# Optimization experiments

Hardware: AMD Instinct MI355X
Metric: run time of the kernel (lower is better)

Reference implementation:

```python
import jax, jax.numpy as jnp
import numpy as np


def setup_inputs() -> dict:
    key = jax.random.key(0)
    ks = jax.random.split(key, 4)
    B, Tq, Tv, D = 8, 256, 512, 256  # decoder_dim = D = 256
    query = jax.random.normal(ks[0], (B, Tq, D), dtype=jnp.float32)
    value = jax.random.normal(ks[1], (B, Tv, D), dtype=jnp.float32)
    W1 = jax.random.normal(ks[2], (D, D), dtype=jnp.float32) * (1.0 / np.sqrt(D))
    b1 = jnp.zeros((D,), dtype=jnp.float32)
    W2 = jax.random.normal(ks[3], (D, D), dtype=jnp.float32) * (1.0 / np.sqrt(D))
    b2 = jnp.zeros((D,), dtype=jnp.float32)
    return {"query": query, "value": value, "W1": W1, "b1": b1, "W2": W2, "b2": b2}


def reference(query, value, W1, b1, W2, b2):
    # Dense projections: [B,Tq,D], [B,Tv,D]
    q = jnp.einsum('bqd,de->bqe', query, W1) + b1
    v = jnp.einsum('bvd,de->bve', value, W2) + b2
    # Additive (Bahdanau) score: broadcast tanh then reduce over feature dim
    # score: [B,Tq,Tv]  (intermediate [B,Tq,Tv,D] is the fusion target)
    score = jnp.tanh(q[:, :, None, :] + v[:, None, :, :]).sum(axis=-1)
    alignment = jax.nn.softmax(score, axis=-1)  # [B,Tq,Tv]
    context = jnp.einsum('bqv,bvd->bqd', alignment, value)  # [B,Tq,D]
    context = jnp.concatenate([context, query], axis=-1)  # [B,Tq,2D]
    alignment_t = jnp.transpose(alignment, (0, 2, 1))  # [B,Tv,Tq]
    return context, alignment_t
```

## Files before the change

### kernel.cpp

```cpp
#include <hip/hip_runtime.h>

#define B_  8
#define TQ  256
#define TV  512
#define DD  256
#define ALGS 520

__device__ __forceinline__ float fast_exp2(float x) {
#if __has_builtin(__builtin_amdgcn_exp2f)
  return __builtin_amdgcn_exp2f(x);
#else
  return __exp2f(x);
#endif
}
__device__ __forceinline__ float fast_rcp(float x) {
#if __has_builtin(__builtin_amdgcn_rcpf)
  return __builtin_amdgcn_rcpf(x);
#else
  return 1.0f / x;
#endif
}

__global__ __launch_bounds__(256) void proj_fused(
    const float* __restrict__ query, const float* __restrict__ value,
    const float* __restrict__ W1, const float* __restrict__ b1,
    const float* __restrict__ W2, const float* __restrict__ b2,
    float* __restrict__ qp, float* __restrict__ vp, float scale) {
  __shared__ float As[2][32][64];
  __shared__ float Bs[2][32][64];
  const int t  = threadIdx.x;
  const int rt = blockIdx.x;
  const int bn = blockIdx.y << 6;

  const float* A; const float* W; const float* bias; float* out; int row0;
  if (rt < 32) { row0 = rt << 6;        A = query; W = W1; bias = b1; out = qp; }
  else         { row0 = (rt - 32) << 6; A = value; W = W2; bias = b2; out = vp; }

  const int tx = t & 15, ty = t >> 4;
  const int aar = t >> 3, aac = (t & 7) << 2;
  const int bbr = t >> 4, bbc = (t & 15) << 2;

  float4 ra[2], rb[2];
#pragma unroll
  for (int it = 0; it < 2; ++it) {
    ra[it] = *(const float4*)(A + (size_t)(row0 + (it << 5) + aar) * DD + aac);
    rb[it] = *(const float4*)(W + (size_t)((it << 4) + bbr) * DD + bn + bbc);
  }
#pragma unroll
  for (int it = 0; it < 2; ++it) {
    const int m = (it << 5) + aar;
#pragma unroll
    for (int c = 0; c < 4; ++c) {
      const int k = aac + c;
      As[0][k][m ^ (((k >> 2) & 7) << 2)] = (&ra[it].x)[c];
    }
    *(float4*)&Bs[0][(it << 4) + bbr][bbc] = rb[it];
  }
  __syncthreads();

  float acc[4][4] = {{0.f,0.f,0.f,0.f},{0.f,0.f,0.f,0.f},
                     {0.f,0.f,0.f,0.f},{0.f,0.f,0.f,0.f}};
  int p = 0;

  for (int k0 = 0; k0 < 256; k0 += 32) {
    const bool more = (k0 + 32) < 256;
    if (more) {
#pragma unroll
      for (int it = 0; it < 2; ++it) {
        ra[it] = *(const float4*)(A + (size_t)(row0 + (it << 5) + aar) * DD + k0 + 32 + aac);
        rb[it] = *(const float4*)(W + (size_t)(k0 + 32 + (it << 4) + bbr) * DD + bn + bbc);
      }
    }
#pragma unroll
    for (int k = 0; k < 32; ++k) {
      float4 aq = *(const float4*)&As[p][k][(ty << 2) ^ (((k >> 2) & 7) << 2)];
      float4 bq = *(const float4*)&Bs[p][k][tx << 2];
      acc[0][0] = fmaf(aq.x, bq.x, acc[0][0]); acc[0][1] = fmaf(aq.x, bq.y, acc[0][1]);
      acc[0][2] = fmaf(aq.x, bq.z, acc[0][2]); acc[0][3] = fmaf(aq.x, bq.w, acc[0][3]);
      acc[1][0] = fmaf(aq.y, bq.x, acc[1][0]); acc[1][1] = fmaf(aq.y, bq.y, acc[1][1]);
      acc[1][2] = fmaf(aq.y, bq.z, acc[1][2]); acc[1][3] = fmaf(aq.y, bq.w, acc[1][3]);
      acc[2][0] = fmaf(aq.z, bq.x, acc[2][0]); acc[2][1] = fmaf(aq.z, bq.y, acc[2][1]);
      acc[2][2] = fmaf(aq.z, bq.z, acc[2][2]); acc[2][3] = fmaf(aq.z, bq.w, acc[2][3]);
      acc[3][0] = fmaf(aq.w, bq.x, acc[3][0]); acc[3][1] = fmaf(aq.w, bq.y, acc[3][1]);
      acc[3][2] = fmaf(aq.w, bq.z, acc[3][2]); acc[3][3] = fmaf(aq.w, bq.w, acc[3][3]);
    }
    if (more) {
      const int q = p ^ 1;
#pragma unroll
      for (int it = 0; it < 2; ++it) {
        const int m = (it << 5) + aar;
#pragma unroll
        for (int c = 0; c < 4; ++c) {
          const int k = aac + c;
          As[q][k][m ^ (((k >> 2) & 7) << 2)] = (&ra[it].x)[c];
        }
        *(float4*)&Bs[q][(it << 4) + bbr][bbc] = rb[it];
      }
      __syncthreads();
      p = q;
    }
  }

  float4 bvv = *(const float4*)&bias[bn + (tx << 2)];
#pragma unroll
  for (int r = 0; r < 4; ++r) {
    float4 o;
    o.x = fast_exp2(scale * (acc[r][0] + bvv.x));
    o.y = fast_exp2(scale * (acc[r][1] + bvv.y));
    o.z = fast_exp2(scale * (acc[r][2] + bvv.z));
    o.w = fast_exp2(scale * (acc[r][3] + bvv.w));
    *(float4*)(out + (size_t)(row0 + (ty << 2) + r) * DD + bn + (tx << 2)) = o;
  }
}

__global__ __launch_bounds__(512, 4) void attn_kernel(
    const float* __restrict__ qp, const float* __restrict__ vp,
    const float* __restrict__ value, const float* __restrict__ query,
    float* __restrict__ out1, float* __restrict__ out2) {
  __shared__ float qs[4 * 256];
  __shared__ float alg[4 * ALGS];
  __shared__ float ctxp[8][4][256];

  const int t    = threadIdx.x;
  const int lane = t & 63;
  const int wv   = t >> 6;
  const int jj   = lane >> 2;
  const int dq   = lane & 3;
  const int bb   = blockIdx.x & 7;
  const int i0   = (blockIdx.x >> 3) << 2;

  const float* vpb = vp + (size_t)bb * TV * DD;
  const float* qb  = qp + (size_t)(bb * TQ + i0) * DD;

  if (t < 256) {
    const int qi = t >> 6, qc = (t & 63) << 2;
    *(float4*)&qs[qi * 256 + qc] = *(const float4*)(qb + (size_t)qi * DD + qc);
  }
  __syncthreads();

  const int jb = (wv << 4) + jj;
  const float* vr0 = vpb + (size_t)jb * DD + (dq << 2);
  const float* vr1 = vr0 + 128 * DD;
  const float* vr2 = vr0 + 256 * DD;
  const float* vr3 = vr0 + 384 * DD;
  const float* qlane = qs + (dq << 2);

  float acc[4][4] = {{0.f,0.f,0.f,0.f},{0.f,0.f,0.f,0.f},
                     {0.f,0.f,0.f,0.f},{0.f,0.f,0.f,0.f}};

#pragma unroll 4
  for (int k = 0; k < 16; ++k) {
    const int doff = k << 4;
    float4 q0 = *(const float4*)(qlane + 0 * 256 + doff);
    float4 q1 = *(const float4*)(qlane + 1 * 256 + doff);
    float4 q2 = *(const float4*)(qlane + 2 * 256 + doff);
    float4 q3 = *(const float4*)(qlane + 3 * 256 + doff);
#pragma unroll
    for (int jg = 0; jg < 4; ++jg) {
      const float* vrp = (jg == 0) ? vr0 : (jg == 1) ? vr1 : (jg == 2) ? vr2 : vr3;
      float4 v4 = *(const float4*)(vrp + doff);
#pragma unroll
      for (int i = 0; i < 4; ++i) {
        const float4 q4 = (i == 0) ? q0 : (i == 1) ? q1 : (i == 2) ? q2 : q3;
        float a = q4.x * v4.x, b = q4.y * v4.y;
        float c = q4.z * v4.z, d = q4.w * v4.w;
        float sab = a + b,  scd = c + d;
        float Q1 = fmaf(a, b, sab + 1.f);
        float Q2 = fmaf(c, d, scd + 1.f);
        float N  = fmaf(scd + 2.f, Q1, (sab + 2.f) * Q2);
        acc[i][jg] = fmaf(N, fast_rcp(Q1 * Q2), acc[i][jg]);
      }
    }
  }

#pragma unroll
  for (int i = 0; i < 4; ++i)
#pragma unroll
    for (int jg = 0; jg < 4; ++jg) {
      acc[i][jg] += __shfl_xor(acc[i][jg], 1, 64);
      acc[i][jg] += __shfl_xor(acc[i][jg], 2, 64);
    }
#pragma unroll
  for (int jg = 0; jg < 4; ++jg) {
    float x = (dq == 0) ? acc[0][jg] : (dq == 1) ? acc[1][jg]
            : (dq == 2) ? acc[2][jg] : acc[3][jg];
    alg[dq * ALGS + (jg << 7) + jb] = x;
  }

  const int f4 = (t & 63) << 2;
  const int s  = t >> 6;
  const float* vb  = value + (size_t)bb * TV * DD;
  const float* vsp = vb + (size_t)(s << 6) * DD + f4;

  float4 pv0 = *(const float4*)(vsp + 0 * DD);
  float4 pv1 = *(const float4*)(vsp + 1 * DD);
  float4 pv2 = *(const float4*)(vsp + 2 * DD);
  float4 pv3 = *(const float4*)(vsp + 3 * DD);

  __syncthreads();

  if (wv < 4) {
    float sv[8];
#pragma unroll
    for (int c = 0; c < 8; ++c) sv[c] = alg[wv * ALGS + (c << 6) + lane];
    float mn = sv[0];
#pragma unroll
    for (int c = 1; c < 8; ++c) mn = fminf(mn, sv[c]);
#pragma unroll
    for (int m = 1; m < 64; m <<= 1) mn = fminf(mn, __shfl_xor(mn, m, 64));

    const float CC = 2.8853900817779268f;
    float p[8];
    float sum = 0.f;
#pragma unroll
    for (int c = 0; c < 8; ++c) { p[c] = fast_exp2(CC * (mn - sv[c])); sum += p[c]; }
#pragma unroll
    for (int m = 1; m < 64; m <<= 1) sum += __shfl_xor(sum, m, 64);
    const float inv = fast_rcp(sum);
#pragma unroll
    for (int c = 0; c < 8; ++c) alg[wv * ALGS + (c << 6) + lane] = p[c] * inv;
  }
  __syncthreads();

  {
    const int j = t;
    float4 av = make_float4(alg[j], alg[ALGS + j], alg[2 * ALGS + j], alg[3 * ALGS + j]);
    *(float4*)(out2 + (size_t)(bb * TV + j) * TQ + i0) = av;
  }

  float c4[4][4] = {{0.f,0.f,0.f,0.f},{0.f,0.f,0.f,0.f},
                    {0.f,0.f,0.f,0.f},{0.f,0.f,0.f,0.f}};
  const int jbase = s << 6;
  {
#pragma unroll
    for (int i = 0; i < 4; ++i) {
      float4 ai = *(const float4*)&alg[i * ALGS + jbase];
      c4[i][0] = fmaf(ai.x, pv0.x, c4[i][0]); c4[i][1] = fmaf(ai.x, pv0.y, c4[i][1]);
      c4[i][2] = fmaf(ai.x, pv0.z, c4[i][2]); c4[i][3] = fmaf(ai.x, pv0.w, c4[i][3]);
      c4[i][0] = fmaf(ai.y, pv1.x, c4[i][0]); c4[i][1] = fmaf(ai.y, pv1.y, c4[i][1]);
      c4[i][2] = fmaf(ai.y, pv1.z, c4[i][2]); c4[i][3] = fmaf(ai.y, pv1.w, c4[i][3]);
      c4[i][0] = fmaf(ai.z, pv2.x, c4[i][0]); c4[i][1] = fmaf(ai.z, pv2.y, c4[i][1]);
      c4[i][2] = fmaf(ai.z, pv2.z, c4[i][2]); c4[i][3] = fmaf(ai.z, pv2.w, c4[i][3]);
      c4[i][0] = fmaf(ai.w, pv3.x, c4[i][0]); c4[i][1] = fmaf(ai.w, pv3.y, c4[i][1]);
      c4[i][2] = fmaf(ai.w, pv3.z, c4[i][2]); c4[i][3] = fmaf(ai.w, pv3.w, c4[i][3]);
    }
  }
#pragma unroll 4
  for (int u = 4; u < 64; u += 4) {
    float4 v0 = *(const float4*)(vsp + (size_t)(u + 0) * DD);
    float4 v1 = *(const float4*)(vsp + (size_t)(u + 1) * DD);
    float4 v2 = *(const float4*)(vsp + (size_t)(u + 2) * DD);
    float4 v3 = *(const float4*)(vsp + (size_t)(u + 3) * DD);
#pragma unroll
    for (int i = 0; i < 4; ++i) {
      float4 ai = *(const float4*)&alg[i * ALGS + jbase + u];
      c4[i][0] = fmaf(ai.x, v0.x, c4[i][0]); c4[i][1] = fmaf(ai.x, v0.y, c4[i][1]);
      c4[i][2] = fmaf(ai.x, v0.z, c4[i][2]); c4[i][3] = fmaf(ai.x, v0.w, c4[i][3]);
      c4[i][0] = fmaf(ai.y, v1.x, c4[i][0]); c4[i][1] = fmaf(ai.y, v1.y, c4[i][1]);
      c4[i][2] = fmaf(ai.y, v1.z, c4[i][2]); c4[i][3] = fmaf(ai.y, v1.w, c4[i][3]);
      c4[i][0] = fmaf(ai.z, v2.x, c4[i][0]); c4[i][1] = fmaf(ai.z, v2.y, c4[i][1]);
      c4[i][2] = fmaf(ai.z, v2.z, c4[i][2]); c4[i][3] = fmaf(ai.z, v2.w, c4[i][3]);
      c4[i][0] = fmaf(ai.w, v3.x, c4[i][0]); c4[i][1] = fmaf(ai.w, v3.y, c4[i][1]);
      c4[i][2] = fmaf(ai.w, v3.z, c4[i][2]); c4[i][3] = fmaf(ai.w, v3.w, c4[i][3]);
    }
  }
#pragma unroll
  for (int i = 0; i < 4; ++i)
    *(float4*)&ctxp[s][i][f4] = make_float4(c4[i][0], c4[i][1], c4[i][2], c4[i][3]);
  __syncthreads();

  const float* qg = query + (size_t)(bb * TQ + i0) * DD;
  float* o = out1 + (size_t)(bb * TQ + i0) * (2 * DD);
#pragma unroll
  for (int it = 0; it < 2; ++it) {
    const int slot = t + (it << 9);
    const int ri = slot >> 8;
    const int ff = slot & 255;
    float sum = 0.f;
#pragma unroll
    for (int ss = 0; ss < 8; ++ss) sum += ctxp[ss][ri][ff];
    o[ri * 512 + ff] = sum;
    o[ri * 512 + 256 + ff] = qg[ri * DD + ff];
  }
}

extern "C" void kernel_launch(void* const* d_in, const int* in_sizes, int n_in,
                              void* d_out, int out_size, void* d_ws, size_t ws_size,
                              hipStream_t stream) {
  const float* query = (const float*)d_in[0];
  const float* value = (const float*)d_in[1];
  const float* W1    = (const float*)d_in[2];
  const float* b1    = (const float*)d_in[3];
  const float* W2    = (const float*)d_in[4];
  const float* b2    = (const float*)d_in[5];

  float* out1 = (float*)d_out;
  float* out2 = out1 + (size_t)B_ * TQ * 2 * DD;

  float* qp = (float*)d_ws;
  float* vp = qp + (size_t)B_ * TQ * DD;

  const float SC = 2.8853900817779268f;

  proj_fused<<<dim3(96, 4), 256, 0, stream>>>(query, value, W1, b1, W2, b2, qp, vp, SC);
  attn_kernel<<<dim3(B_ * (TQ / 4)), 512, 0, stream>>>(qp, vp, value, query, out1, out2);
}
```

Measured before the change: 130.9 us.

## Split score computation over feature halves into separate kernel for more parallelism

The fused attention kernel is split in two. The first kernel computes partial tanh-sum scores over half of the feature dimension, using 1024 blocks and a higher occupancy hint, and writes them to workspace. The second kernel sums the two halves, applies softmax and computes the context. The aim is to double the block count for the compute-heavy score phase so that all CUs are filled. The cost is an extra launch plus a partial-score round trip through global memory, and the old monolithic kernel is kept as a fallback when the workspace is too small.

```diff
diff --git a/kernel.cpp b/kernel.cpp
--- a/kernel.cpp
+++ b/kernel.cpp
@@ -113,33 +113,33 @@
   }
 }
 
-__global__ __launch_bounds__(512, 4) void attn_kernel(
+__global__ __launch_bounds__(512, 8) void score_part(
     const float* __restrict__ qp, const float* __restrict__ vp,
-    const float* __restrict__ value, const float* __restrict__ query,
-    float* __restrict__ out1, float* __restrict__ out2) {
-  __shared__ float qs[4 * 256];
+    float* __restrict__ Sp) {
+  __shared__ float qs[4 * 128];
   __shared__ float alg[4 * ALGS];
-  __shared__ float ctxp[8][4][256];
 
   const int t    = threadIdx.x;
   const int lane = t & 63;
   const int wv   = t >> 6;
   const int jj   = lane >> 2;
   const int dq   = lane & 3;
-  const int bb   = blockIdx.x & 7;
-  const int i0   = (blockIdx.x >> 3) << 2;
+  const int bx   = blockIdx.x;
+  const int bb   = bx & 7;
+  const int rest = bx >> 3;
+  const int iblk = rest & 63;
+  const int i0   = iblk << 2;
+  const int dh   = rest >> 6;
+  const int d0   = dh << 7;
 
   const float* vpb = vp + (size_t)bb * TV * DD;
-  const float* qb  = qp + (size_t)(bb * TQ + i0) * DD;
-
-  if (t < 256) {
-    const int qi = t >> 6, qc = (t & 63) << 2;
-    *(float4*)&qs[qi * 256 + qc] = *(const float4*)(qb + (size_t)qi * DD + qc);
-  }
+  const float* qb  = qp + (size_t)(bb * TQ + i0) * DD + d0;
+
+  qs[t] = qb[(size_t)(t >> 7) * DD + (t & 127)];
   __syncthreads();
 
   const int jb = (wv << 4) + jj;
-  const float* vr0 = vpb + (size_t)jb * DD + (dq << 2);
+  const float* vr0 = vpb + (size_t)jb * DD + d0 + (dq << 2);
   const float* vr1 = vr0 + 128 * DD;
   const float* vr2 = vr0 + 256 * DD;
   const float* vr3 = vr0 + 384 * DD;
@@ -149,12 +149,12 @@
                      {0.f,0.f,0.f,0.f},{0.f,0.f,0.f,0.f}};
 
 #pragma unroll 4
-  for (int k = 0; k < 16; ++k) {
+  for (int k = 0; k < 8; ++k) {
     const int doff = k << 4;
-    float4 q0 = *(const float4*)(qlane + 0 * 256 + doff);
-    float4 q1 = *(const float4*)(qlane + 1 * 256 + doff);
-    float4 q2 = *(const float4*)(qlane + 2 * 256 + doff);
-    float4 q3 = *(const float4*)(qlane + 3 * 256 + doff);
+    float4 q0 = *(const float4*)(qlane + 0 * 128 + doff);
+    float4 q1 = *(const float4*)(qlane + 1 * 128 + doff);
+    float4 q2 = *(const float4*)(qlane + 2 * 128 + doff);
+    float4 q3 = *(const float4*)(qlane + 3 * 128 + doff);
 #pragma unroll
     for (int jg = 0; jg < 4; ++jg) {
       const float* vrp = (jg == 0) ? vr0 : (jg == 1) ? vr1 : (jg == 2) ? vr2 : vr3;
@@ -186,6 +186,29 @@
             : (dq == 2) ? acc[2][jg] : acc[3][jg];
     alg[dq * ALGS + (jg << 7) + jb] = x;
   }
+  __syncthreads();
+
+  float* sb = Sp + ((size_t)(dh * 8 + bb) * 64 + iblk) * (4 * 512);
+  const int r = t >> 7, c = (t & 127) << 2;
+  *(float4*)(sb + r * 512 + c) = *(const float4*)&alg[r * ALGS + c];
+}
+
+__global__ __launch_bounds__(512, 4) void attn_ctx(
+    const float* __restrict__ Sp, const float* __restrict__ value,
+    const float* __restrict__ query, float* __restrict__ out1,
+    float* __restrict__ out2) {
+  __shared__ float alg[4 * ALGS];
+  __shared__ float ctxp[8][4][256];
+
+  const int t    = threadIdx.x;
+  const int lane = t & 63;
+  const int wv   = t >> 6;
+  const int bb   = blockIdx.x & 7;
+  const int iblk = blockIdx.x >> 3;
+  const int i0   = iblk << 2;
+
+  const float* slo = Sp + ((size_t)(0 * 8 + bb) * 64 + iblk) * (4 * 512);
+  const float* shi = Sp + ((size_t)(1 * 8 + bb) * 64 + iblk) * (4 * 512);
 
   const int f4 = (t & 63) << 2;
   const int s  = t >> 6;
@@ -197,12 +220,11 @@
   float4 pv2 = *(const float4*)(vsp + 2 * DD);
   float4 pv3 = *(const float4*)(vsp + 3 * DD);
 
-  __syncthreads();
-
   if (wv < 4) {
     float sv[8];
 #pragma unroll
-    for (int c = 0; c < 8; ++c) sv[c] = alg[wv * ALGS + (c << 6) + lane];
+    for (int c = 0; c < 8; ++c)
+      sv[c] = slo[wv * 512 + (c << 6) + lane] + shi[wv * 512 + (c << 6) + lane];
     float mn = sv[0];
 #pragma unroll
     for (int c = 1; c < 8; ++c) mn = fminf(mn, sv[c]);
@@ -284,6 +306,177 @@
   }
 }
 
+__global__ __launch_bounds__(512, 4) void attn_mono(
+    const float* __restrict__ qp, const float* __restrict__ vp,
+    const float* __restrict__ value, const float* __restrict__ query,
+    float* __restrict__ out1, float* __restrict__ out2) {
+  __shared__ float qs[4 * 256];
+  __shared__ float alg[4 * ALGS];
+  __shared__ float ctxp[8][4][256];
+
+  const int t    = threadIdx.x;
+  const int lane = t & 63;
+  const int wv   = t >> 6;
+  const int jj   = lane >> 2;
+  const int dq   = lane & 3;
+  const int bb   = blockIdx.x & 7;
+  const int i0   = (blockIdx.x >> 3) << 2;
+
+  const float* vpb = vp + (size_t)bb * TV * DD;
+  const float* qb  = qp + (size_t)(bb * TQ + i0) * DD;
+
+  if (t < 256) {
+    const int qi = t >> 6, qc = (t & 63) << 2;
+    *(float4*)&qs[qi * 256 + qc] = *(const float4*)(qb + (size_t)qi * DD + qc);
+  }
+  __syncthreads();
+
+  const int jb = (wv << 4) + jj;
+  const float* vr0 = vpb + (size_t)jb * DD + (dq << 2);
+  const float* vr1 = vr0 + 128 * DD;
+  const float* vr2 = vr0 + 256 * DD;
+  const float* vr3 = vr0 + 384 * DD;
+  const float* qlane = qs + (dq << 2);
+
+  float acc[4][4] = {{0.f,0.f,0.f,0.f},{0.f,0.f,0.f,0.f},
+                     {0.f,0.f,0.f,0.f},{0.f,0.f,0.f,0.f}};
+
+#pragma unroll 4
+  for (int k = 0; k < 16; ++k) {
+    const int doff = k << 4;
+    float4 q0 = *(const float4*)(qlane + 0 * 256 + doff);
+    float4 q1 = *(const float4*)(qlane + 1 * 256 + doff);
+    float4 q2 = *(const float4*)(qlane + 2 * 256 + doff);
+    float4 q3 = *(const float4*)(qlane + 3 * 256 + doff);
+#pragma unroll
+    for (int jg = 0; jg < 4; ++jg) {
+      const float* vrp = (jg == 0) ? vr0 : (jg == 1) ? vr1 : (jg == 2) ? vr2 : vr3;
+      float4 v4 = *(const float4*)(vrp + doff);
+#pragma unroll
+      for (int i = 0; i < 4; ++i) {
+        const float4 q4 = (i == 0) ? q0 : (i == 1) ? q1 : (i == 2) ? q2 : q3;
+        float a = q4.x * v4.x, b = q4.y * v4.y;
+        float c = q4.z * v4.z, d = q4.w * v4.w;
+        float sab = a + b,  scd = c + d;
+        float Q1 = fmaf(a, b, sab + 1.f);
+        float Q2 = fmaf(c, d, scd + 1.f);
+        float N  = fmaf(scd + 2.f, Q1, (sab + 2.f) * Q2);
+        acc[i][jg] = fmaf(N, fast_rcp(Q1 * Q2), acc[i][jg]);
+      }
+    }
+  }
+
+#pragma unroll
+  for (int i = 0; i < 4; ++i)
+#pragma unroll
+    for (int jg = 0; jg < 4; ++jg) {
+      acc[i][jg] += __shfl_xor(acc[i][jg], 1, 64);
+      acc[i][jg] += __shfl_xor(acc[i][jg], 2, 64);
+    }
+#pragma unroll
+  for (int jg = 0; jg < 4; ++jg) {
+    float x = (dq == 0) ? acc[0][jg] : (dq == 1) ? acc[1][jg]
+            : (dq == 2) ? acc[2][jg] : acc[3][jg];
+    alg[dq * ALGS + (jg << 7) + jb] = x;
+  }
+
+  const int f4 = (t & 63) << 2;
+  const int s  = t >> 6;
+  const float* vb  = value + (size_t)bb * TV * DD;
+  const float* vsp = vb + (size_t)(s << 6) * DD + f4;
+
+  float4 pv0 = *(const float4*)(vsp + 0 * DD);
+  float4 pv1 = *(const float4*)(vsp + 1 * DD);
+  float4 pv2 = *(const float4*)(vsp + 2 * DD);
+  float4 pv3 = *(const float4*)(vsp + 3 * DD);
+
+  __syncthreads();
+
+  if (wv < 4) {
+    float sv[8];
+#pragma unroll
+    for (int c = 0; c < 8; ++c) sv[c] = alg[wv * ALGS + (c << 6) + lane];
+    float mn = sv[0];
+#pragma unroll
+    for (int c = 1; c < 8; ++c) mn = fminf(mn, sv[c]);
+#pragma unroll
+    for (int m = 1; m < 64; m <<= 1) mn = fminf(mn, __shfl_xor(mn, m, 64));
+
+    const float CC = 2.8853900817779268f;
+    float p[8];
+    float sum = 0.f;
+#pragma unroll
+    for (int c = 0; c < 8; ++c) { p[c] = fast_exp2(CC * (mn - sv[c])); sum += p[c]; }
+#pragma unroll
+    for (int m = 1; m < 64; m <<= 1) sum += __shfl_xor(sum, m, 64);
+    const float inv = fast_rcp(sum);
+#pragma unroll
+    for (int c = 0; c < 8; ++c) alg[wv * ALGS + (c << 6) + lane] = p[c] * inv;
+  }
+  __syncthreads();
+
+  {
+    const int j = t;
+    float4 av = make_float4(alg[j], alg[ALGS + j], alg[2 * ALGS + j], alg[3 * ALGS + j]);
+    *(float4*)(out2 + (size_t)(bb * TV + j) * TQ + i0) = av;
+  }
+
+  float c4[4][4] = {{0.f,0.f,0.f,0.f},{0.f,0.f,0.f,0.f},
+                    {0.f,0.f,0.f,0.f},{0.f,0.f,0.f,0.f}};
+  const int jbase = s << 6;
+  {
+#pragma unroll
+    for (int i = 0; i < 4; ++i) {
+      float4 ai = *(const float4*)&alg[i * ALGS + jbase];
+      c4[i][0] = fmaf(ai.x, pv0.x, c4[i][0]); c4[i][1] = fmaf(ai.x, pv0.y, c4[i][1]);
+      c4[i][2] = fmaf(ai.x, pv0.z, c4[i][2]); c4[i][3] = fmaf(ai.x, pv0.w, c4[i][3]);
+      c4[i][0] = fmaf(ai.y, pv1.x, c4[i][0]); c4[i][1] = fmaf(ai.y, pv1.y, c4[i][1]);
+      c4[i][2] = fmaf(ai.y, pv1.z, c4[i][2]); c4[i][3] = fmaf(ai.y, pv1.w, c4[i][3]);
+      c4[i][0] = fmaf(ai.z, pv2.x, c4[i][0]); c4[i][1] = fmaf(ai.z, pv2.y, c4[i][1]);
+      c4[i][2] = fmaf(ai.z, pv2.z, c4[i][2]); c4[i][3] = fmaf(ai.z, pv2.w, c4[i][3]);
+      c4[i][0] = fmaf(ai.w, pv3.x, c4[i][0]); c4[i][1] = fmaf(ai.w, pv3.y, c4[i][1]);
+      c4[i][2] = fmaf(ai.w, pv3.z, c4[i][2]); c4[i][3] = fmaf(ai.w, pv3.w, c4[i][3]);
+    }
+  }
+#pragma unroll 4
+  for (int u = 4; u < 64; u += 4) {
+    float4 v0 = *(const float4*)(vsp + (size_t)(u + 0) * DD);
+    float4 v1 = *(const float4*)(vsp + (size_t)(u + 1) * DD);
+    float4 v2 = *(const float4*)(vsp + (size_t)(u + 2) * DD);
+    float4 v3 = *(const float4*)(vsp + (size_t)(u + 3) * DD);
+#pragma unroll
+    for (int i = 0; i < 4; ++i) {
+      float4 ai = *(const float4*)&alg[i * ALGS + jbase + u];
+      c4[i][0] = fmaf(ai.x, v0.x, c4[i][0]); c4[i][1] = fmaf(ai.x, v0.y, c4[i][1]);
+      c4[i][2] = fmaf(ai.x, v0.z, c4[i][2]); c4[i][3] = fmaf(ai.x, v0.w, c4[i][3]);
+      c4[i][0] = fmaf(ai.y, v1.x, c4[i][0]); c4[i][1] = fmaf(ai.y, v1.y, c4[i][1]);
+      c4[i][2] = fmaf(ai.y, v1.z, c4[i][2]); c4[i][3] = fmaf(ai.y, v1.w, c4[i][3]);
+      c4[i][0] = fmaf(ai.z, v2.x, c4[i][0]); c4[i][1] = fmaf(ai.z, v2.y, c4[i][1]);
+      c4[i][2] = fmaf(ai.z, v2.z, c4[i][2]); c4[i][3] = fmaf(ai.z, v2.w, c4[i][3]);
+      c4[i][0] = fmaf(ai.w, v3.x, c4[i][0]); c4[i][1] = fmaf(ai.w, v3.y, c4[i][1]);
+      c4[i][2] = fmaf(ai.w, v3.z, c4[i][2]); c4[i][3] = fmaf(ai.w, v3.w, c4[i][3]);
+    }
+  }
+#pragma unroll
+  for (int i = 0; i < 4; ++i)
+    *(float4*)&ctxp[s][i][f4] = make_float4(c4[i][0], c4[i][1], c4[i][2], c4[i][3]);
+  __syncthreads();
+
+  const float* qg = query + (size_t)(bb * TQ + i0) * DD;
+  float* o = out1 + (size_t)(bb * TQ + i0) * (2 * DD);
+#pragma unroll
+  for (int it = 0; it < 2; ++it) {
+    const int slot = t + (it << 9);
+    const int ri = slot >> 8;
+    const int ff = slot & 255;
+    float sum = 0.f;
+#pragma unroll
+    for (int ss = 0; ss < 8; ++ss) sum += ctxp[ss][ri][ff];
+    o[ri * 512 + ff] = sum;
+    o[ri * 512 + 256 + ff] = qg[ri * DD + ff];
+  }
+}
+
 extern "C" void kernel_launch(void* const* d_in, const int* in_sizes, int n_in,
                               void* d_out, int out_size, void* d_ws, size_t ws_size,
                               hipStream_t stream) {
@@ -299,9 +492,19 @@
 
   float* qp = (float*)d_ws;
   float* vp = qp + (size_t)B_ * TQ * DD;
+  float* Sp = vp + (size_t)B_ * TV * DD;
+
+  const size_t need = ((size_t)B_ * TQ * DD + (size_t)B_ * TV * DD +
+                       (size_t)2 * 8 * 64 * 4 * 512) * sizeof(float);
 
   const float SC = 2.8853900817779268f;
 
   proj_fused<<<dim3(96, 4), 256, 0, stream>>>(query, value, W1, b1, W2, b2, qp, vp, SC);
-  attn_kernel<<<dim3(B_ * (TQ / 4)), 512, 0, stream>>>(qp, vp, value, query, out1, out2);
-}
+
+  if (ws_size >= need) {
+    score_part<<<dim3(1024), 512, 0, stream>>>(qp, vp, Sp);
+    attn_ctx<<<dim3(512), 512, 0, stream>>>(Sp, value, query, out1, out2);
+  } else {
+    attn_mono<<<dim3(B_ * (TQ / 4)), 512, 0, stream>>>(qp, vp, value, query, out1, out2);
+  }
+}
```

Result: no change. 132.6 us (+1.3%).
